# Optimization experiments

Hardware: AMD Instinct MI355X
Metric: run time of the kernel (lower is better)

## Reference

```python
import jax, jax.numpy as jnp
import numpy as np

N, M = 2048, 2048
NODE_DIM = 64
HIDDEN_DIM = 64  # must equal NODE_DIM due to broadcast in msg = weights * h_r
LN_EPS = 1e-5


def setup_inputs() -> dict:
    key = jax.random.key(0)
    ks = jax.random.split(key, 14)
    s_edge1 = 1.0 / np.sqrt(4.0)
    s_edge2 = 1.0 / np.sqrt(HIDDEN_DIM)
    s_n1 = 1.0 / np.sqrt(NODE_DIM + HIDDEN_DIM)
    s_n2 = 1.0 / np.sqrt(NODE_DIM)
    return {
        "h_l": jax.random.normal(ks[0], (N, NODE_DIM), jnp.float32),
        "x_l": jax.random.normal(ks[1], (N, 3), jnp.float32),
        "h_r": jax.random.normal(ks[2], (M, NODE_DIM), jnp.float32),
        "x_r": jax.random.normal(ks[3], (M, 3), jnp.float32),
        # edge_mlp: Linear(4, hidden), SiLU, Linear(hidden, hidden)
        "W1": jax.random.uniform(ks[4], (4, HIDDEN_DIM), jnp.float32, -s_edge1, s_edge1),
        "b1": jax.random.uniform(ks[5], (HIDDEN_DIM,), jnp.float32, -s_edge1, s_edge1),
        "W2": jax.random.uniform(ks[6], (HIDDEN_DIM, HIDDEN_DIM), jnp.float32, -s_edge2, s_edge2),
        "b2": jax.random.uniform(ks[7], (HIDDEN_DIM,), jnp.float32, -s_edge2, s_edge2),
        # node_update: Linear(node+hidden, node), LayerNorm(node), SiLU, Linear(node, node)
        "Wn1": jax.random.uniform(ks[8], (NODE_DIM + HIDDEN_DIM, NODE_DIM), jnp.float32, -s_n1, s_n1),
        "bn1": jax.random.uniform(ks[9], (NODE_DIM,), jnp.float32, -s_n1, s_n1),
        "ln_g": jnp.ones((NODE_DIM,), jnp.float32),
        "ln_b": jnp.zeros((NODE_DIM,), jnp.float32),
        "Wn2": jax.random.uniform(ks[10], (NODE_DIM, NODE_DIM), jnp.float32, -s_n2, s_n2),
        "bn2": jax.random.uniform(ks[11], (NODE_DIM,), jnp.float32, -s_n2, s_n2),
    }


def _forward(h_l, x_l, h_r, x_r, W1, b1, W2, b2, Wn1, bn1, ln_g, ln_b, Wn2, bn2):
    # squared pairwise distances [N, M]
    d2 = jnp.sum((x_l[:, None, :] - x_r[None, :, :]) ** 2, axis=-1)
    dist_feat = jnp.exp(-d2 / 5.0)
    # chemical-property interaction matrices from last 3 node features
    l_p, r_p = h_l[:, -3:], h_r[:, -3:]
    hbond = l_p[:, 0:1] * r_p[:, 1:2].T + l_p[:, 1:2] * r_p[:, 0:1].T  # [N, M]
    hydro = l_p[:, 2:3] * r_p[:, 2:3].T                                # [N, M]
    edge_raw = jnp.stack([dist_feat, hbond, hydro, jnp.ones_like(d2)], axis=-1)  # [N, M, 4]
    # edge MLP -> sigmoid gating weights [N, M, H]
    e = jax.nn.silu(edge_raw @ W1 + b1) @ W2 + b2
    w = jax.nn.sigmoid(e)
    # weighted, normalized aggregation over M
    h_agg = jnp.einsum('nmh,mh->nh', w, h_r) / (jnp.sum(w, axis=1) + 1e-6)
    # node update MLP with LayerNorm
    z = jnp.concatenate([h_l, h_agg], axis=-1) @ Wn1 + bn1
    mu = jnp.mean(z, axis=-1, keepdims=True)
    var = jnp.var(z, axis=-1, keepdims=True)
    z = (z - mu) / jnp.sqrt(var + LN_EPS) * ln_g + ln_b
    z = jax.nn.silu(z) @ Wn2 + bn2
    return h_l + z


def reference(h_l, x_l, h_r, x_r, W1, b1, W2, b2, Wn1, bn1, ln_g, ln_b, Wn2, bn2):
    return _forward(h_l, x_l, h_r, x_r, W1, b1, W2, b2, Wn1, bn1, ln_g, ln_b, Wn2, bn2)
```

## Files before the change

kernel.cpp:

```cpp
#include <hip/hip_runtime.h>
#include <hip/hip_bf16.h>

#define NTOT 2048
#define MTOT 2048
#define MSPLIT 16
#define MCHUNK 64

typedef short bf16x8 __attribute__((ext_vector_type(8)));
typedef float f32x4  __attribute__((ext_vector_type(4)));
typedef int   i32x4  __attribute__((ext_vector_type(4)));

#define NL2E (-1.4426950408889634f)
#define C1E  (-0.2885390081777927f)

__device__ __forceinline__ float fast_exp2(float x) {
#if __has_builtin(__builtin_amdgcn_exp2f)
  return __builtin_amdgcn_exp2f(x);
#else
  return __exp2f(x);
#endif
}
__device__ __forceinline__ float fast_rcp(float x) {
#if __has_builtin(__builtin_amdgcn_rcpf)
  return __builtin_amdgcn_rcpf(x);
#else
  return 1.0f / x;
#endif
}
__device__ __forceinline__ float fast_rsq(float x) {
#if __has_builtin(__builtin_amdgcn_rsqf)
  return __builtin_amdgcn_rsqf(x);
#else
  return rsqrtf(x);
#endif
}

__device__ __forceinline__ float ldf(const __hip_bfloat16* p, int i) {
  return __bfloat162float(p[i]);
}
__device__ __forceinline__ float ldf(const float* p, int i) { return p[i]; }

__device__ __forceinline__ short to_bf16_rne(float x) {
  union { float f; unsigned u; } v; v.f = x;
  unsigned r = v.u + 0x7FFFu + ((v.u >> 16) & 1u);
  return (short)(r >> 16);
}
__device__ __forceinline__ short ldbf(const __hip_bfloat16* p, int i) {
  return ((const short*)p)[i];
}
__device__ __forceinline__ short ldbf(const float* p, int i) {
  return to_bf16_rne(p[i]);
}

__device__ __forceinline__ void stf(__hip_bfloat16* p, int i, float v) {
  p[i] = __float2bfloat16(v);
}
__device__ __forceinline__ void stf(float* p, int i, float v) { p[i] = v; }

__device__ __forceinline__ unsigned pack_bf16_rn(float lo, float hi) {
  union { float f; unsigned u; } a, b;
  a.f = lo; b.f = hi;
  unsigned au = a.u + 0x8000u, bu = b.u + 0x8000u;
#if __has_builtin(__builtin_amdgcn_perm)
  return __builtin_amdgcn_perm(bu, au, 0x07060302u);
#else
  return (au >> 16) | (bu & 0xffff0000u);
#endif
}

__device__ __forceinline__ int sniff_is_f32(const void* hl) {
  const unsigned short* p = (const unsigned short*)hl;
#pragma unroll 1
  for (int i = 0; i < 128; ++i) {
    unsigned u = ((unsigned)p[i]) << 16;
    float f = __builtin_bit_cast(float, u);
    if (!(fabsf(f) <= 1e3f)) return 1;
  }
  return 0;
}

template <typename T, bool WANT_F32>
__global__ __launch_bounds__(256, 2)
void edge_kernel(const T* __restrict__ h_l,
                 const T* __restrict__ x_l,
                 const T* __restrict__ h_r,
                 const T* __restrict__ x_r,
                 const T* __restrict__ W1,
                 const T* __restrict__ b1,
                 const T* __restrict__ W2,
                 const T* __restrict__ b2,
                 float* __restrict__ num_g,
                 float* __restrict__ den_g) {
  if (sniff_is_f32(h_l) != (WANT_F32 ? 1 : 0)) return;

  __shared__ float hr_s[MCHUNK][64];
  __shared__ float xr_s[MCHUNK][8];

  const int tid  = threadIdx.x;
  const int wave = tid >> 6;
  const int lane = tid & 63;
  const int l15  = lane & 15;
  const int quad = lane >> 4;

  const int nblk   = blockIdx.x / MSPLIT;
  const int msplit = blockIdx.x % MSPLIT;
  const int n0     = nblk * 64 + wave * 16;
  const int mPer   = MTOT / MSPLIT;
  const int mBase  = msplit * mPer;

  const int nA = n0 + l15;
  const float xl0 = ldf(x_l, nA * 3 + 0);
  const float xl1 = ldf(x_l, nA * 3 + 1);
  const float xl2 = ldf(x_l, nA * 3 + 2);
  const float lp0 = ldf(h_l, nA * 64 + 61);
  const float lp1 = ldf(h_l, nA * 64 + 62);
  const float lp2 = ldf(h_l, nA * 64 + 63);

  float w1d[16], w1h[16], w1y[16], b1p[16];
#pragma unroll
  for (int j = 0; j < 8; ++j) {
    const int ha = quad * 8 + j, hb = 32 + quad * 8 + j;
    w1d[j] = ldf(W1, 0 * 64 + ha);   w1d[8 + j] = ldf(W1, 0 * 64 + hb);
    w1h[j] = ldf(W1, 1 * 64 + ha);   w1h[8 + j] = ldf(W1, 1 * 64 + hb);
    w1y[j] = ldf(W1, 2 * 64 + ha);   w1y[8 + j] = ldf(W1, 2 * 64 + hb);
    b1p[j]     = ldf(b1, ha) + ldf(W1, 3 * 64 + ha);
    b1p[8 + j] = ldf(b1, hb) + ldf(W1, 3 * 64 + hb);
  }

  bf16x8 Bfrag[4][2];
#pragma unroll
  for (int c = 0; c < 4; ++c) {
#pragma unroll
    for (int h = 0; h < 2; ++h) {
      bf16x8 f;
#pragma unroll
      for (int j = 0; j < 8; ++j) {
        const int k = h * 32 + quad * 8 + j;
        f[j] = ldbf(W2, k * 64 + c * 16 + l15);
      }
      Bfrag[c][h] = f;
    }
  }

  float b2c[4];
#pragma unroll
  for (int c = 0; c < 4; ++c) b2c[c] = NL2E * ldf(b2, c * 16 + l15);

  const f32x4 zero4 = {0.f, 0.f, 0.f, 0.f};
  float numr[4][4], denr[4][4];
#pragma unroll
  for (int c = 0; c < 4; ++c)
#pragma unroll
    for (int r = 0; r < 4; ++r) { numr[c][r] = 0.f; denr[c][r] = 0.f; }

  for (int mc = 0; mc < mPer; mc += MCHUNK) {
    __syncthreads();
    for (int idx = tid; idx < MCHUNK * 64; idx += 256) {
      const int mm = idx >> 6, hh = idx & 63;
      hr_s[mm][hh] = ldf(h_r, (mBase + mc + mm) * 64 + hh);
    }
    for (int idx = tid; idx < MCHUNK * 8; idx += 256) {
      const int mm = idx >> 3, k = idx & 7;
      float v = 0.f;
      const int m = mBase + mc + mm;
      if (k < 3)      v = ldf(x_r, m * 3 + k);
      else if (k < 6) v = ldf(h_r, m * 64 + 61 + (k - 3));
      xr_s[mm][k] = v;
    }
    __syncthreads();

#pragma unroll 1
    for (int ms = 0; ms < MCHUNK; ++ms) {
      const float xr0 = xr_s[ms][0], xr1 = xr_s[ms][1], xr2 = xr_s[ms][2];
      const float rp0 = xr_s[ms][3], rp1 = xr_s[ms][4], rp2 = xr_s[ms][5];
      const float dx = xl0 - xr0, dy = xl1 - xr1, dz = xl2 - xr2;
      const float d2 = fmaf(dz, dz, fmaf(dy, dy, dx * dx));
      const float dist = fast_exp2(d2 * C1E);
      const float hb = fmaf(lp1, rp0, lp0 * rp1);
      const float hy = lp2 * rp2;

      float s[16];
#pragma unroll
      for (int j = 0; j < 16; ++j) {
        const float t = fmaf(dist, w1d[j], fmaf(hb, w1h[j], fmaf(hy, w1y[j], b1p[j])));
        s[j] = t * fast_rcp(1.0f + fast_exp2(t * NL2E));
      }
      i32x4 p0, p1;
      p0.x = pack_bf16_rn(s[0], s[1]);   p0.y = pack_bf16_rn(s[2], s[3]);
      p0.z = pack_bf16_rn(s[4], s[5]);   p0.w = pack_bf16_rn(s[6], s[7]);
      p1.x = pack_bf16_rn(s[8], s[9]);   p1.y = pack_bf16_rn(s[10], s[11]);
      p1.z = pack_bf16_rn(s[12], s[13]); p1.w = pack_bf16_rn(s[14], s[15]);
      const bf16x8 A0 = __builtin_bit_cast(bf16x8, p0);
      const bf16x8 A1 = __builtin_bit_cast(bf16x8, p1);

      f32x4 acc[4];
#pragma unroll
      for (int c = 0; c < 4; ++c) {
        acc[c] = __builtin_amdgcn_mfma_f32_16x16x32_bf16(A0, Bfrag[c][0], zero4, 0, 0, 0);
        acc[c] = __builtin_amdgcn_mfma_f32_16x16x32_bf16(A1, Bfrag[c][1], acc[c], 0, 0, 0);
      }

#pragma unroll
      for (int c = 0; c < 4; ++c) {
        const float hrv = hr_s[ms][c * 16 + l15];
#pragma unroll
        for (int r = 0; r < 4; ++r) {
          const float w = fast_rcp(1.0f + fast_exp2(fmaf(acc[c][r], NL2E, b2c[c])));
          numr[c][r] = fmaf(w, hrv, numr[c][r]);
          denr[c][r] += w;
        }
      }
    }
  }

#pragma unroll
  for (int c = 0; c < 4; ++c)
#pragma unroll
    for (int r = 0; r < 4; ++r) {
      const int n = n0 + quad * 4 + r;
      const int h2 = c * 16 + l15;
      atomicAdd(&num_g[n * 64 + h2], numr[c][r]);
      atomicAdd(&den_g[n * 64 + h2], denr[c][r]);
    }
}

template <typename T, bool WANT_F32>
__global__ __launch_bounds__(256)
void node_kernel(const T* __restrict__ h_l,
                 const float* __restrict__ num_g,
                 const float* __restrict__ den_g,
                 const T* __restrict__ Wn1,
                 const T* __restrict__ bn1,
                 const T* __restrict__ ln_g,
                 const T* __restrict__ ln_b,
                 const T* __restrict__ Wn2,
                 const T* __restrict__ bn2,
                 T* __restrict__ out) {
  if (sniff_is_f32(h_l) != (WANT_F32 ? 1 : 0)) return;

  __shared__ float Wn1_s[128 * 64];
  __shared__ float Wn2_s[64 * 64];
  __shared__ float xbuf[4][128];
  __shared__ float zbuf[4][64];

  const int tid = threadIdx.x;
  for (int i = tid; i < 128 * 64; i += 256) Wn1_s[i] = ldf(Wn1, i);
  for (int i = tid; i < 64 * 64; i += 256) Wn2_s[i] = ldf(Wn2, i);

  const int wave = tid >> 6, lane = tid & 63;
  const int row = blockIdx.x * 4 + wave;

  const float hl = ldf(h_l, row * 64 + lane);
  const float dn = den_g[row * 64 + lane] + 1e-6f;
  const float hagg = num_g[row * 64 + lane] * fast_rcp(dn);
  xbuf[wave][lane] = hl;
  xbuf[wave][64 + lane] = hagg;
  __syncthreads();

  float t = ldf(bn1, lane);
#pragma unroll 8
  for (int k = 0; k < 128; ++k) t = fmaf(xbuf[wave][k], Wn1_s[k * 64 + lane], t);

  float s1 = t, s2 = t * t;
#pragma unroll
  for (int off = 32; off; off >>= 1) {
    s1 += __shfl_xor(s1, off);
    s2 += __shfl_xor(s2, off);
  }
  const float mu = s1 * 0.015625f;
  const float var = fmaf(s2, 0.015625f, -mu * mu);
  const float rs = fast_rsq(var + 1e-5f);
  const float zn = fmaf((t - mu) * rs, ldf(ln_g, lane), ldf(ln_b, lane));
  const float sz = zn * fast_rcp(1.0f + fast_exp2(zn * NL2E));
  zbuf[wave][lane] = sz;
  __syncthreads();

  float o = ldf(bn2, lane);
#pragma unroll 8
  for (int k = 0; k < 64; ++k) o = fmaf(zbuf[wave][k], Wn2_s[k * 64 + lane], o);

  stf(out, row * 64 + lane, hl + o);
}

extern "C" void kernel_launch(void* const* d_in, const int* in_sizes, int n_in,
                              void* d_out, int out_size, void* d_ws, size_t ws_size,
                              hipStream_t stream) {
  float* num_g = (float*)d_ws;
  float* den_g = num_g + (size_t)NTOT * 64;

  hipMemsetAsync(d_ws, 0, (size_t)NTOT * 64 * 2 * sizeof(float), stream);

  const dim3 egrid((NTOT / 64) * MSPLIT), eblk(256);
  const dim3 ngrid(NTOT / 4), nblk2(256);

  {
    typedef __hip_bfloat16 T;
    edge_kernel<T, false><<<egrid, eblk, 0, stream>>>(
        (const T*)d_in[0], (const T*)d_in[1], (const T*)d_in[2], (const T*)d_in[3],
        (const T*)d_in[4], (const T*)d_in[5], (const T*)d_in[6], (const T*)d_in[7],
        num_g, den_g);
    node_kernel<T, false><<<ngrid, nblk2, 0, stream>>>(
        (const T*)d_in[0], num_g, den_g,
        (const T*)d_in[8], (const T*)d_in[9], (const T*)d_in[10], (const T*)d_in[11],
        (const T*)d_in[12], (const T*)d_in[13], (T*)d_out);
  }
  {
    typedef float T;
    edge_kernel<T, true><<<egrid, eblk, 0, stream>>>(
        (const T*)d_in[0], (const T*)d_in[1], (const T*)d_in[2], (const T*)d_in[3],
        (const T*)d_in[4], (const T*)d_in[5], (const T*)d_in[6], (const T*)d_in[7],
        num_g, den_g);
    node_kernel<T, true><<<ngrid, nblk2, 0, stream>>>(
        (const T*)d_in[0], num_g, den_g,
        (const T*)d_in[8], (const T*)d_in[9], (const T*)d_in[10], (const T*)d_in[11],
        (const T*)d_in[12], (const T*)d_in[13], (T*)d_out);
  }
}
```

Before: 251.9 us.

## Drop dtype-sniffing dual launches and split the edge kernel one M-chunk per block

Removes the runtime dtype sniff and the duplicate bf16/f32 kernel launches, so only the f32 edge and node kernels run. This drops two early-exit launches and a serial 128-element scan at the start of every thread. The edge kernel now uses MSPLIT=32, so each block processes exactly one 64-wide M chunk: the outer chunk loop and its barriers go away, and the grid doubles. Launch bounds are raised to 4 blocks per CU. In exchange, global atomic traffic for the partial sums doubles and register pressure is tighter.

```diff
diff --git a/kernel.cpp b/kernel.cpp
--- a/kernel.cpp
+++ b/kernel.cpp
@@ -1,9 +1,10 @@
 #include <hip/hip_runtime.h>
 #include <hip/hip_bf16.h>
 
+
 #define NTOT 2048
 #define MTOT 2048
-#define MSPLIT 16
+#define MSPLIT 32
 #define MCHUNK 64
 
 typedef short bf16x8 __attribute__((ext_vector_type(8)));
@@ -34,28 +35,12 @@
   return rsqrtf(x);
 #endif
 }
-
-__device__ __forceinline__ float ldf(const __hip_bfloat16* p, int i) {
-  return __bfloat162float(p[i]);
-}
-__device__ __forceinline__ float ldf(const float* p, int i) { return p[i]; }
 
 __device__ __forceinline__ short to_bf16_rne(float x) {
   union { float f; unsigned u; } v; v.f = x;
   unsigned r = v.u + 0x7FFFu + ((v.u >> 16) & 1u);
   return (short)(r >> 16);
 }
-__device__ __forceinline__ short ldbf(const __hip_bfloat16* p, int i) {
-  return ((const short*)p)[i];
-}
-__device__ __forceinline__ short ldbf(const float* p, int i) {
-  return to_bf16_rne(p[i]);
-}
-
-__device__ __forceinline__ void stf(__hip_bfloat16* p, int i, float v) {
-  p[i] = __float2bfloat16(v);
-}
-__device__ __forceinline__ void stf(float* p, int i, float v) { p[i] = v; }
 
 __device__ __forceinline__ unsigned pack_bf16_rn(float lo, float hi) {
   union { float f; unsigned u; } a, b;
@@ -68,31 +53,17 @@
 #endif
 }
 
-__device__ __forceinline__ int sniff_is_f32(const void* hl) {
-  const unsigned short* p = (const unsigned short*)hl;
-#pragma unroll 1
-  for (int i = 0; i < 128; ++i) {
-    unsigned u = ((unsigned)p[i]) << 16;
-    float f = __builtin_bit_cast(float, u);
-    if (!(fabsf(f) <= 1e3f)) return 1;
-  }
-  return 0;
-}
-
-template <typename T, bool WANT_F32>
-__global__ __launch_bounds__(256, 2)
-void edge_kernel(const T* __restrict__ h_l,
-                 const T* __restrict__ x_l,
-                 const T* __restrict__ h_r,
-                 const T* __restrict__ x_r,
-                 const T* __restrict__ W1,
-                 const T* __restrict__ b1,
-                 const T* __restrict__ W2,
-                 const T* __restrict__ b2,
+__global__ __launch_bounds__(256, 4)
+void edge_kernel(const float* __restrict__ h_l,
+                 const float* __restrict__ x_l,
+                 const float* __restrict__ h_r,
+                 const float* __restrict__ x_r,
+                 const float* __restrict__ W1,
+                 const float* __restrict__ b1,
+                 const float* __restrict__ W2,
+                 const float* __restrict__ b2,
                  float* __restrict__ num_g,
                  float* __restrict__ den_g) {
-  if (sniff_is_f32(h_l) != (WANT_F32 ? 1 : 0)) return;
-
   __shared__ float hr_s[MCHUNK][64];
   __shared__ float xr_s[MCHUNK][8];
 
@@ -105,26 +76,25 @@
   const int nblk   = blockIdx.x / MSPLIT;
   const int msplit = blockIdx.x % MSPLIT;
   const int n0     = nblk * 64 + wave * 16;
-  const int mPer   = MTOT / MSPLIT;
-  const int mBase  = msplit * mPer;
+  const int mBase  = msplit * MCHUNK;
 
   const int nA = n0 + l15;
-  const float xl0 = ldf(x_l, nA * 3 + 0);
-  const float xl1 = ldf(x_l, nA * 3 + 1);
-  const float xl2 = ldf(x_l, nA * 3 + 2);
-  const float lp0 = ldf(h_l, nA * 64 + 61);
-  const float lp1 = ldf(h_l, nA * 64 + 62);
-  const float lp2 = ldf(h_l, nA * 64 + 63);
+  const float xl0 = x_l[nA * 3 + 0];
+  const float xl1 = x_l[nA * 3 + 1];
+  const float xl2 = x_l[nA * 3 + 2];
+  const float lp0 = h_l[nA * 64 + 61];
+  const float lp1 = h_l[nA * 64 + 62];
+  const float lp2 = h_l[nA * 64 + 63];
 
   float w1d[16], w1h[16], w1y[16], b1p[16];
 #pragma unroll
   for (int j = 0; j < 8; ++j) {
     const int ha = quad * 8 + j, hb = 32 + quad * 8 + j;
-    w1d[j] = ldf(W1, 0 * 64 + ha);   w1d[8 + j] = ldf(W1, 0 * 64 + hb);
-    w1h[j] = ldf(W1, 1 * 64 + ha);   w1h[8 + j] = ldf(W1, 1 * 64 + hb);
-    w1y[j] = ldf(W1, 2 * 64 + ha);   w1y[8 + j] = ldf(W1, 2 * 64 + hb);
-    b1p[j]     = ldf(b1, ha) + ldf(W1, 3 * 64 + ha);
-    b1p[8 + j] = ldf(b1, hb) + ldf(W1, 3 * 64 + hb);
+    w1d[j] = W1[0 * 64 + ha];   w1d[8 + j] = W1[0 * 64 + hb];
+    w1h[j] = W1[1 * 64 + ha];   w1h[8 + j] = W1[1 * 64 + hb];
+    w1y[j] = W1[2 * 64 + ha];   w1y[8 + j] = W1[2 * 64 + hb];
+    b1p[j]     = b1[ha] + W1[3 * 64 + ha];
+    b1p[8 + j] = b1[hb] + W1[3 * 64 + hb];
   }
 
   bf16x8 Bfrag[4][2];
@@ -136,7 +106,7 @@
 #pragma unroll
       for (int j = 0; j < 8; ++j) {
         const int k = h * 32 + quad * 8 + j;
-        f[j] = ldbf(W2, k * 64 + c * 16 + l15);
+        f[j] = to_bf16_rne(W2[k * 64 + c * 16 + l15]);
       }
       Bfrag[c][h] = f;
     }
@@ -144,7 +114,20 @@
 
   float b2c[4];
 #pragma unroll
-  for (int c = 0; c < 4; ++c) b2c[c] = NL2E * ldf(b2, c * 16 + l15);
+  for (int c = 0; c < 4; ++c) b2c[c] = NL2E * b2[c * 16 + l15];
+
+  for (int idx = tid; idx < MCHUNK * 64; idx += 256) {
+    const int mm = idx >> 6, hh = idx & 63;
+    hr_s[mm][hh] = h_r[(mBase + mm) * 64 + hh];
+  }
+  for (int idx = tid; idx < MCHUNK * 8; idx += 256) {
+    const int mm = idx >> 3, k = idx & 7;
+    float v = 0.f;
+    const int m = mBase + mm;
+    if (k < 3)      v = x_r[m * 3 + k];
+    else if (k < 6) v = h_r[m * 64 + 61 + (k - 3)];
+    xr_s[mm][k] = v;
+  }
 
   const f32x4 zero4 = {0.f, 0.f, 0.f, 0.f};
   float numr[4][4], denr[4][4];
@@ -153,62 +136,47 @@
 #pragma unroll
     for (int r = 0; r < 4; ++r) { numr[c][r] = 0.f; denr[c][r] = 0.f; }
 
-  for (int mc = 0; mc < mPer; mc += MCHUNK) {
-    __syncthreads();
-    for (int idx = tid; idx < MCHUNK * 64; idx += 256) {
-      const int mm = idx >> 6, hh = idx & 63;
-      hr_s[mm][hh] = ldf(h_r, (mBase + mc + mm) * 64 + hh);
-    }
-    for (int idx = tid; idx < MCHUNK * 8; idx += 256) {
-      const int mm = idx >> 3, k = idx & 7;
-      float v = 0.f;
-      const int m = mBase + mc + mm;
-      if (k < 3)      v = ldf(x_r, m * 3 + k);
-      else if (k < 6) v = ldf(h_r, m * 64 + 61 + (k - 3));
-      xr_s[mm][k] = v;
-    }
-    __syncthreads();
+  __syncthreads();
 
 #pragma unroll 1
-    for (int ms = 0; ms < MCHUNK; ++ms) {
-      const float xr0 = xr_s[ms][0], xr1 = xr_s[ms][1], xr2 = xr_s[ms][2];
-      const float rp0 = xr_s[ms][3], rp1 = xr_s[ms][4], rp2 = xr_s[ms][5];
-      const float dx = xl0 - xr0, dy = xl1 - xr1, dz = xl2 - xr2;
-      const float d2 = fmaf(dz, dz, fmaf(dy, dy, dx * dx));
-      const float dist = fast_exp2(d2 * C1E);
-      const float hb = fmaf(lp1, rp0, lp0 * rp1);
-      const float hy = lp2 * rp2;
-
-      float s[16];
-#pragma unroll
-      for (int j = 0; j < 16; ++j) {
-        const float t = fmaf(dist, w1d[j], fmaf(hb, w1h[j], fmaf(hy, w1y[j], b1p[j])));
-        s[j] = t * fast_rcp(1.0f + fast_exp2(t * NL2E));
-      }
-      i32x4 p0, p1;
-      p0.x = pack_bf16_rn(s[0], s[1]);   p0.y = pack_bf16_rn(s[2], s[3]);
-      p0.z = pack_bf16_rn(s[4], s[5]);   p0.w = pack_bf16_rn(s[6], s[7]);
-      p1.x = pack_bf16_rn(s[8], s[9]);   p1.y = pack_bf16_rn(s[10], s[11]);
-      p1.z = pack_bf16_rn(s[12], s[13]); p1.w = pack_bf16_rn(s[14], s[15]);
-      const bf16x8 A0 = __builtin_bit_cast(bf16x8, p0);
-      const bf16x8 A1 = __builtin_bit_cast(bf16x8, p1);
-
-      f32x4 acc[4];
-#pragma unroll
-      for (int c = 0; c < 4; ++c) {
-        acc[c] = __builtin_amdgcn_mfma_f32_16x16x32_bf16(A0, Bfrag[c][0], zero4, 0, 0, 0);
-        acc[c] = __builtin_amdgcn_mfma_f32_16x16x32_bf16(A1, Bfrag[c][1], acc[c], 0, 0, 0);
-      }
-
-#pragma unroll
-      for (int c = 0; c < 4; ++c) {
-        const float hrv = hr_s[ms][c * 16 + l15];
-#pragma unroll
-        for (int r = 0; r < 4; ++r) {
-          const float w = fast_rcp(1.0f + fast_exp2(fmaf(acc[c][r], NL2E, b2c[c])));
-          numr[c][r] = fmaf(w, hrv, numr[c][r]);
-          denr[c][r] += w;
-        }
+  for (int ms = 0; ms < MCHUNK; ++ms) {
+    const float xr0 = xr_s[ms][0], xr1 = xr_s[ms][1], xr2 = xr_s[ms][2];
+    const float rp0 = xr_s[ms][3], rp1 = xr_s[ms][4], rp2 = xr_s[ms][5];
+    const float dx = xl0 - xr0, dy = xl1 - xr1, dz = xl2 - xr2;
+    const float d2 = fmaf(dz, dz, fmaf(dy, dy, dx * dx));
+    const float dist = fast_exp2(d2 * C1E);
+    const float hb = fmaf(lp1, rp0, lp0 * rp1);
+    const float hy = lp2 * rp2;
+
+    float s[16];
+#pragma unroll
+    for (int j = 0; j < 16; ++j) {
+      const float t = fmaf(dist, w1d[j], fmaf(hb, w1h[j], fmaf(hy, w1y[j], b1p[j])));
+      s[j] = t * fast_rcp(1.0f + fast_exp2(t * NL2E));
+    }
+    i32x4 p0, p1;
+    p0.x = pack_bf16_rn(s[0], s[1]);   p0.y = pack_bf16_rn(s[2], s[3]);
+    p0.z = pack_bf16_rn(s[4], s[5]);   p0.w = pack_bf16_rn(s[6], s[7]);
+    p1.x = pack_bf16_rn(s[8], s[9]);   p1.y = pack_bf16_rn(s[10], s[11]);
+    p1.z = pack_bf16_rn(s[12], s[13]); p1.w = pack_bf16_rn(s[14], s[15]);
+    const bf16x8 A0 = __builtin_bit_cast(bf16x8, p0);
+    const bf16x8 A1 = __builtin_bit_cast(bf16x8, p1);
+
+    f32x4 acc[4];
+#pragma unroll
+    for (int c = 0; c < 4; ++c) {
+      acc[c] = __builtin_amdgcn_mfma_f32_16x16x32_bf16(A0, Bfrag[c][0], zero4, 0, 0, 0);
+      acc[c] = __builtin_amdgcn_mfma_f32_16x16x32_bf16(A1, Bfrag[c][1], acc[c], 0, 0, 0);
+    }
+
+#pragma unroll
+    for (int c = 0; c < 4; ++c) {
+      const float hrv = hr_s[ms][c * 16 + l15];
+#pragma unroll
+      for (int r = 0; r < 4; ++r) {
+        const float w = fast_rcp(1.0f + fast_exp2(fmaf(acc[c][r], NL2E, b2c[c])));
+        numr[c][r] = fmaf(w, hrv, numr[c][r]);
+        denr[c][r] += w;
       }
     }
   }
@@ -224,40 +192,37 @@
     }
 }
 
-template <typename T, bool WANT_F32>
 __global__ __launch_bounds__(256)
-void node_kernel(const T* __restrict__ h_l,
+void node_kernel(const float* __restrict__ h_l,
                  const float* __restrict__ num_g,
                  const float* __restrict__ den_g,
-                 const T* __restrict__ Wn1,
-                 const T* __restrict__ bn1,
-                 const T* __restrict__ ln_g,
-                 const T* __restrict__ ln_b,
-                 const T* __restrict__ Wn2,
-                 const T* __restrict__ bn2,
-                 T* __restrict__ out) {
-  if (sniff_is_f32(h_l) != (WANT_F32 ? 1 : 0)) return;
-
+                 const float* __restrict__ Wn1,
+                 const float* __restrict__ bn1,
+                 const float* __restrict__ ln_g,
+                 const float* __restrict__ ln_b,
+                 const float* __restrict__ Wn2,
+                 const float* __restrict__ bn2,
+                 float* __restrict__ out) {
   __shared__ float Wn1_s[128 * 64];
   __shared__ float Wn2_s[64 * 64];
   __shared__ float xbuf[4][128];
   __shared__ float zbuf[4][64];
 
   const int tid = threadIdx.x;
-  for (int i = tid; i < 128 * 64; i += 256) Wn1_s[i] = ldf(Wn1, i);
-  for (int i = tid; i < 64 * 64; i += 256) Wn2_s[i] = ldf(Wn2, i);
+  for (int i = tid; i < 128 * 64; i += 256) Wn1_s[i] = Wn1[i];
+  for (int i = tid; i < 64 * 64; i += 256) Wn2_s[i] = Wn2[i];
 
   const int wave = tid >> 6, lane = tid & 63;
   const int row = blockIdx.x * 4 + wave;
 
-  const float hl = ldf(h_l, row * 64 + lane);
+  const float hl = h_l[row * 64 + lane];
   const float dn = den_g[row * 64 + lane] + 1e-6f;
   const float hagg = num_g[row * 64 + lane] * fast_rcp(dn);
   xbuf[wave][lane] = hl;
   xbuf[wave][64 + lane] = hagg;
   __syncthreads();
 
-  float t = ldf(bn1, lane);
+  float t = bn1[lane];
 #pragma unroll 8
   for (int k = 0; k < 128; ++k) t = fmaf(xbuf[wave][k], Wn1_s[k * 64 + lane], t);
 
@@ -270,49 +235,42 @@
   const float mu = s1 * 0.015625f;
   const float var = fmaf(s2, 0.015625f, -mu * mu);
   const float rs = fast_rsq(var + 1e-5f);
-  const float zn = fmaf((t - mu) * rs, ldf(ln_g, lane), ldf(ln_b, lane));
+  const float zn = fmaf((t - mu) * rs, ln_g[lane], ln_b[lane]);
   const float sz = zn * fast_rcp(1.0f + fast_exp2(zn * NL2E));
   zbuf[wave][lane] = sz;
   __syncthreads();
 
-  float o = ldf(bn2, lane);
+  float o = bn2[lane];
 #pragma unroll 8
   for (int k = 0; k < 64; ++k) o = fmaf(zbuf[wave][k], Wn2_s[k * 64 + lane], o);
 
-  stf(out, row * 64 + lane, hl + o);
+  out[row * 64 + lane] = hl + o;
 }
 
 extern "C" void kernel_launch(void* const* d_in, const int* in_sizes, int n_in,
                               void* d_out, int out_size, void* d_ws, size_t ws_size,
                               hipStream_t stream) {
+  const float* h_l = (const float*)d_in[0];
+  const float* x_l = (const float*)d_in[1];
+  const float* h_r = (const float*)d_in[2];
+  const float* x_r = (const float*)d_in[3];
+  const float* W1  = (const float*)d_in[4];
+  const float* b1  = (const float*)d_in[5];
+  const float* W2  = (const float*)d_in[6];
+  const float* b2  = (const float*)d_in[7];
+  const float* Wn1 = (const float*)d_in[8];
+  const float* bn1 = (const float*)d_in[9];
+  const float* lng = (const float*)d_in[10];
+  const float* lnb = (const float*)d_in[11];
+  const float* Wn2 = (const float*)d_in[12];
+  const float* bn2 = (const float*)d_in[13];
+
   float* num_g = (float*)d_ws;
   float* den_g = num_g + (size_t)NTOT * 64;
 
   hipMemsetAsync(d_ws, 0, (size_t)NTOT * 64 * 2 * sizeof(float), stream);
-
-  const dim3 egrid((NTOT / 64) * MSPLIT), eblk(256);
-  const dim3 ngrid(NTOT / 4), nblk2(256);
-
-  {
-    typedef __hip_bfloat16 T;
-    edge_kernel<T, false><<<egrid, eblk, 0, stream>>>(
-        (const T*)d_in[0], (const T*)d_in[1], (const T*)d_in[2], (const T*)d_in[3],
-        (const T*)d_in[4], (const T*)d_in[5], (const T*)d_in[6], (const T*)d_in[7],
-        num_g, den_g);
-    node_kernel<T, false><<<ngrid, nblk2, 0, stream>>>(
-        (const T*)d_in[0], num_g, den_g,
-        (const T*)d_in[8], (const T*)d_in[9], (const T*)d_in[10], (const T*)d_in[11],
-        (const T*)d_in[12], (const T*)d_in[13], (T*)d_out);
-  }
-  {
-    typedef float T;
-    edge_kernel<T, true><<<egrid, eblk, 0, stream>>>(
-        (const T*)d_in[0], (const T*)d_in[1], (const T*)d_in[2], (const T*)d_in[3],
-        (const T*)d_in[4], (const T*)d_in[5], (const T*)d_in[6], (const T*)d_in[7],
-        num_g, den_g);
-    node_kernel<T, true><<<ngrid, nblk2, 0, stream>>>(
-        (const T*)d_in[0], num_g, den_g,
-        (const T*)d_in[8], (const T*)d_in[9], (const T*)d_in[10], (const T*)d_in[11],
-        (const T*)d_in[12], (const T*)d_in[13], (T*)d_out);
-  }
-}
+  edge_kernel<<<dim3((NTOT / 64) * MSPLIT), dim3(256), 0, stream>>>(
+      h_l, x_l, h_r, x_r, W1, b1, W2, b2, num_g, den_g);
+  node_kernel<<<dim3(NTOT / 4), dim3(256), 0, stream>>>(
+      h_l, num_g, den_g, Wn1, bn1, lng, lnb, Wn2, bn2, (float*)d_out);
+}
```

Result: slower. 541.5 us (+115.0%).
